# Performance work log

Measured on AMD Instinct MI355X. Metric: run time of the kernel, lower is better.

## Reference

```python
import jax, jax.numpy as jnp
import numpy as np

WS = 8          # window_size
NH = 8          # num_heads


def rel_pos_index(ws):
    coords = jnp.stack(jnp.meshgrid(jnp.arange(ws), jnp.arange(ws), indexing='ij'))  # [2,ws,ws]
    cf = coords.reshape(2, -1)                      # [2, N]
    rc = (cf[:, :, None] - cf[:, None, :]).transpose(1, 2, 0)  # [N,N,2]
    rc = rc + (ws - 1)
    return rc[..., 0] * (2 * ws - 1) + rc[..., 1]   # [N,N] int


def setup_inputs() -> dict:
    key = jax.random.key(0)
    ks = jax.random.split(key, 10)
    dim = 256
    B_, N = 4096, WS * WS
    nW = 1024
    return {
        'ref': jax.random.normal(ks[0], (B_, N, dim), jnp.float32),
        'adj': jax.random.normal(ks[1], (B_, N, dim), jnp.float32),
        'mask': jax.random.normal(ks[2], (nW, N, N), jnp.float32),
        'q_w': jax.random.normal(ks[3], (dim, dim), jnp.float32) * 0.02,
        'q_b': jax.random.normal(ks[4], (dim,), jnp.float32) * 0.02,
        'kv_w': jax.random.normal(ks[5], (2 * dim, dim), jnp.float32) * 0.02,
        'kv_b': jax.random.normal(ks[6], (2 * dim,), jnp.float32) * 0.02,
        'proj_w': jax.random.normal(ks[7], (dim, dim), jnp.float32) * 0.02,
        'proj_b': jax.random.normal(ks[8], (dim,), jnp.float32) * 0.02,
        'rpb_table': jax.random.normal(ks[9], ((2 * WS - 1) ** 2, NH), jnp.float32) * 0.02,
        'H': 256,
        'W': 256,
    }


def reference(ref, adj, mask, q_w, q_b, kv_w, kv_b, proj_w, proj_b, rpb_table, H, W):
    B_, N, C = ref.shape
    hd = C // NH
    scale = hd ** -0.5
    # projections (torch Linear: x @ W.T + b)
    q = (ref @ q_w.T + q_b).reshape(B_, N, NH, hd).transpose(0, 2, 1, 3)    # [B_,h,N,d]
    kv = (adj @ kv_w.T + kv_b).reshape(B_, N, 2, NH, hd)
    k = kv[:, :, 0].transpose(0, 2, 1, 3)                                   # [B_,h,N,d]
    v = kv[:, :, 1].transpose(0, 2, 1, 3)
    attn = jnp.einsum('bhnd,bhmd->bhnm', q * scale, k)                      # [B_,h,N,N]
    # relative position bias gather
    rpi = rel_pos_index(WS)                                                 # [N,N]
    bias = rpb_table[rpi.reshape(-1)].reshape(N, N, NH).transpose(2, 0, 1)  # [h,N,N]
    attn = attn + bias[None]
    # shifted-window mask
    nW = (H // WS) * (W // WS)
    attn = attn.reshape(B_ // nW, nW, NH, N, N) + mask[None, :, None]
    attn = attn.reshape(B_, NH, N, N)
    attn = jax.nn.softmax(attn, axis=-1)
    out = jnp.einsum('bhnm,bhmd->bhnd', attn, v).transpose(0, 2, 1, 3).reshape(B_, N, C)
    return out @ proj_w.T + proj_b
```

## Files before the change

### kernel.cpp

```cpp
#include <hip/hip_runtime.h>

typedef unsigned short u16;
typedef unsigned int u32;
typedef float f32x4 __attribute__((ext_vector_type(4)));
typedef __bf16 bf16x8 __attribute__((ext_vector_type(8)));

__device__ __forceinline__ u32 pack2(float a, float b) {
  u32 r;
  asm("v_cvt_pk_bf16_f32 %0, %1, %2" : "=v"(r) : "v"(a), "v"(b));
  return r;
}

__device__ __forceinline__ bf16x8 xpose_tile(const f32x4 t0, const f32x4 t1,
                                             int srcA, int srcB, bool hi) {
  u32 s0 = pack2(t0[0], t0[1]);
  u32 s1 = pack2(t0[2], t0[3]);
  u32 s2 = pack2(t1[0], t1[1]);
  u32 s3 = pack2(t1[2], t1[3]);
  u32 a00 = (u32)__shfl((int)s0, srcA), a20 = (u32)__shfl((int)s2, srcA);
  u32 a01 = (u32)__shfl((int)s1, srcA), a21 = (u32)__shfl((int)s3, srcA);
  u32 b00 = (u32)__shfl((int)s0, srcB), b20 = (u32)__shfl((int)s2, srcB);
  u32 b01 = (u32)__shfl((int)s1, srcB), b21 = (u32)__shfl((int)s3, srcB);
  uint4 u;
  u.x = hi ? a20 : a00;
  u.y = hi ? a21 : a01;
  u.z = hi ? b20 : b00;
  u.w = hi ? b21 : b01;
  return __builtin_bit_cast(bf16x8, u);
}

__global__ void prep_kern(const float* __restrict__ qw_f, const float* __restrict__ kvw_f,
                          const float* __restrict__ pjw_f, const float* __restrict__ rpb,
                          const float* __restrict__ mask_g,
                          uint4* __restrict__ qwt, uint4* __restrict__ kwt,
                          uint4* __restrict__ vwt, uint4* __restrict__ pjwt,
                          float4* __restrict__ biasT, float4* __restrict__ maskT, int nW) {
  int i = blockIdx.x * 256 + threadIdx.x;
  auto wxf = [&](const float* W, int ro, int idx, uint4* dst) {
    int l = idx & 63, kk = (idx >> 6) & 7, R = idx >> 9;
    const float* s = W + (ro + R * 16 + (l & 15)) * 256 + kk * 32 + 8 * (l >> 4);
    uint4 o;
    o.x = pack2(s[0], s[1]);
    o.y = pack2(s[2], s[3]);
    o.z = pack2(s[4], s[5]);
    o.w = pack2(s[6], s[7]);
    dst[idx] = o;
  };
  if (i < 32768) {
    wxf(qw_f, 0, i, qwt);
  } else if (i < 65536) {
    wxf(kvw_f, 0, i - 32768, kwt);
  } else if (i < 98304) {
    wxf(kvw_f, 256, i - 65536, vwt);
  } else if (i < 131072) {
    wxf(pjw_f, 0, i - 98304, pjwt);
  } else if (i < 139264) {
    int j = i - 131072;
    int l = j & 63, mt = (j >> 6) & 3, nt = (j >> 8) & 3, h = j >> 10;
    int n = nt * 16 + (l & 15), m0 = mt * 16 + 4 * (l >> 4);
    float4 o;
    float* po = (float*)&o;
#pragma unroll
    for (int e = 0; e < 4; ++e) {
      int m = m0 + e;
      int rp = ((n >> 3) - (m >> 3) + 7) * 15 + ((n & 7) - (m & 7) + 7);
      po[e] = rpb[rp * 8 + h];
    }
    biasT[j] = o;
  } else {
    int k = i - 139264;
    if (k < nW * 1024) {
      int l = k & 63, mt = (k >> 6) & 3, nt = (k >> 8) & 3, wd = k >> 10;
      int n = nt * 16 + (l & 15), m0 = mt * 16 + 4 * (l >> 4);
      maskT[k] = *(const float4*)(mask_g + (size_t)wd * 4096 + n * 64 + m0);
    }
  }
}

#define XROW 528

#define K1_LDS 67584

__global__ __launch_bounds__(256, 2) void winattn_kern(
    const float* __restrict__ xr_g, const float* __restrict__ xa_g,
    const float* __restrict__ qb_g, const float* __restrict__ kvb_g,
    const float* __restrict__ pb_g,
    const uint4* __restrict__ qwt, const uint4* __restrict__ kwt,
    const uint4* __restrict__ vwt, const uint4* __restrict__ pjwt,
    const float4* __restrict__ biasT, const float4* __restrict__ maskT,
    float* __restrict__ out_g, int nW) {
  extern __shared__ char smem[];
  const int tid = threadIdx.x;
  const int l = tid & 63, wv = tid >> 6;
  const int lr = l & 15, lq = l >> 4;
  const int b = blockIdx.x;
  const int wd = b % nW;
  const float scale = 0.17677669529663687f;
  const int srcA = lr + 32 * (lq & 1);
  const int srcB = srcA + 16;
  const bool hi = (lq >> 1) != 0;

  {
    const float* refb = xr_g + (size_t)b * 16384;
    const float* adjb = xa_g + (size_t)b * 16384;
#pragma unroll 4
    for (int it = 0; it < 16; ++it) {
      int flat = it * 256 + tid;
      int t = flat >> 6, c4 = (flat & 63) << 2;
      float4 vr = *(const float4*)(refb + t * 256 + c4);
      float4 va = *(const float4*)(adjb + t * 256 + c4);
      uint2 wr_, wa_;
      wr_.x = pack2(vr.x, vr.y);
      wr_.y = pack2(vr.z, vr.w);
      wa_.x = pack2(va.x, va.y);
      wa_.y = pack2(va.z, va.w);
      *(uint2*)(smem + t * XROW + c4 * 2) = wr_;
      *(uint2*)(smem + 33792 + t * XROW + c4 * 2) = wa_;
    }
  }
  __syncthreads();

  bf16x8 bfr[2][4], afr[2][4];

  {
    f32x4 qacc[4][4];
#pragma unroll
    for (int i = 0; i < 4; ++i)
#pragma unroll
      for (int j = 0; j < 4; ++j) qacc[i][j] = {0.f, 0.f, 0.f, 0.f};
#pragma unroll 2
    for (int kk = 0; kk < 8; ++kk) {
      bf16x8 a0 = *(const bf16x8*)&qwt[((wv * 4 + 0) * 8 + kk) * 64 + l];
      bf16x8 a1 = *(const bf16x8*)&qwt[((wv * 4 + 1) * 8 + kk) * 64 + l];
      bf16x8 a2 = *(const bf16x8*)&qwt[((wv * 4 + 2) * 8 + kk) * 64 + l];
      bf16x8 a3 = *(const bf16x8*)&qwt[((wv * 4 + 3) * 8 + kk) * 64 + l];
      int c = kk * 32 + 8 * lq;
#pragma unroll
      for (int nt = 0; nt < 4; ++nt) {
        bf16x8 bt = *(const bf16x8*)(smem + (nt * 16 + lr) * XROW + c * 2);
        qacc[0][nt] = __builtin_amdgcn_mfma_f32_16x16x32_bf16(a0, bt, qacc[0][nt], 0, 0, 0);
        qacc[1][nt] = __builtin_amdgcn_mfma_f32_16x16x32_bf16(a1, bt, qacc[1][nt], 0, 0, 0);
        qacc[2][nt] = __builtin_amdgcn_mfma_f32_16x16x32_bf16(a2, bt, qacc[2][nt], 0, 0, 0);
        qacc[3][nt] = __builtin_amdgcn_mfma_f32_16x16x32_bf16(a3, bt, qacc[3][nt], 0, 0, 0);
      }
    }
#pragma unroll
    for (int rt = 0; rt < 4; ++rt) {
      float4 b4 = *(const float4*)(qb_g + wv * 64 + rt * 16 + 4 * lq);
#pragma unroll
      for (int nt = 0; nt < 4; ++nt) {
        qacc[rt][nt][0] = (qacc[rt][nt][0] + b4.x) * scale;
        qacc[rt][nt][1] = (qacc[rt][nt][1] + b4.y) * scale;
        qacc[rt][nt][2] = (qacc[rt][nt][2] + b4.z) * scale;
        qacc[rt][nt][3] = (qacc[rt][nt][3] + b4.w) * scale;
      }
    }
#pragma unroll
    for (int h2 = 0; h2 < 2; ++h2)
#pragma unroll
      for (int nt = 0; nt < 4; ++nt)
        bfr[h2][nt] = xpose_tile(qacc[2 * h2][nt], qacc[2 * h2 + 1][nt], srcA, srcB, hi);
  }
  __syncthreads();

  {
    f32x4 kacc[4][4];
#pragma unroll
    for (int i = 0; i < 4; ++i)
#pragma unroll
      for (int j = 0; j < 4; ++j) kacc[i][j] = {0.f, 0.f, 0.f, 0.f};
#pragma unroll 2
    for (int kk = 0; kk < 8; ++kk) {
      bf16x8 a0 = *(const bf16x8*)&kwt[((wv * 4 + 0) * 8 + kk) * 64 + l];
      bf16x8 a1 = *(const bf16x8*)&kwt[((wv * 4 + 1) * 8 + kk) * 64 + l];
      bf16x8 a2 = *(const bf16x8*)&kwt[((wv * 4 + 2) * 8 + kk) * 64 + l];
      bf16x8 a3 = *(const bf16x8*)&kwt[((wv * 4 + 3) * 8 + kk) * 64 + l];
      int c = kk * 32 + 8 * lq;
#pragma unroll
      for (int nt = 0; nt < 4; ++nt) {
        bf16x8 bt = *(const bf16x8*)(smem + 33792 + (nt * 16 + lr) * XROW + c * 2);
        kacc[0][nt] = __builtin_amdgcn_mfma_f32_16x16x32_bf16(a0, bt, kacc[0][nt], 0, 0, 0);
        kacc[1][nt] = __builtin_amdgcn_mfma_f32_16x16x32_bf16(a1, bt, kacc[1][nt], 0, 0, 0);
        kacc[2][nt] = __builtin_amdgcn_mfma_f32_16x16x32_bf16(a2, bt, kacc[2][nt], 0, 0, 0);
        kacc[3][nt] = __builtin_amdgcn_mfma_f32_16x16x32_bf16(a3, bt, kacc[3][nt], 0, 0, 0);
      }
    }
#pragma unroll
    for (int rt = 0; rt < 4; ++rt) {
      float4 b4 = *(const float4*)(kvb_g + wv * 64 + rt * 16 + 4 * lq);
#pragma unroll
      for (int nt = 0; nt < 4; ++nt) {
        kacc[rt][nt][0] += b4.x;
        kacc[rt][nt][1] += b4.y;
        kacc[rt][nt][2] += b4.z;
        kacc[rt][nt][3] += b4.w;
      }
    }
#pragma unroll
    for (int h2 = 0; h2 < 2; ++h2)
#pragma unroll
      for (int nt = 0; nt < 4; ++nt)
        afr[h2][nt] = xpose_tile(kacc[2 * h2][nt], kacc[2 * h2 + 1][nt], srcA, srcB, hi);
  }

  bf16x8 vfr[2][2][2];
  {
    f32x4 vacc[4][4];
#pragma unroll
    for (int i = 0; i < 4; ++i)
#pragma unroll
      for (int j = 0; j < 4; ++j) vacc[i][j] = {0.f, 0.f, 0.f, 0.f};
#pragma unroll 2
    for (int kk = 0; kk < 8; ++kk) {
      bf16x8 b0 = *(const bf16x8*)&vwt[((wv * 4 + 0) * 8 + kk) * 64 + l];
      bf16x8 b1 = *(const bf16x8*)&vwt[((wv * 4 + 1) * 8 + kk) * 64 + l];
      bf16x8 b2 = *(const bf16x8*)&vwt[((wv * 4 + 2) * 8 + kk) * 64 + l];
      bf16x8 b3 = *(const bf16x8*)&vwt[((wv * 4 + 3) * 8 + kk) * 64 + l];
      int c = kk * 32 + 8 * lq;
#pragma unroll
      for (int mt = 0; mt < 4; ++mt) {
        bf16x8 at = *(const bf16x8*)(smem + 33792 + (mt * 16 + lr) * XROW + c * 2);
        vacc[mt][0] = __builtin_amdgcn_mfma_f32_16x16x32_bf16(at, b0, vacc[mt][0], 0, 0, 0);
        vacc[mt][1] = __builtin_amdgcn_mfma_f32_16x16x32_bf16(at, b1, vacc[mt][1], 0, 0, 0);
        vacc[mt][2] = __builtin_amdgcn_mfma_f32_16x16x32_bf16(at, b2, vacc[mt][2], 0, 0, 0);
        vacc[mt][3] = __builtin_amdgcn_mfma_f32_16x16x32_bf16(at, b3, vacc[mt][3], 0, 0, 0);
      }
    }
#pragma unroll
    for (int ct = 0; ct < 4; ++ct) {
      float bv = kvb_g[256 + wv * 64 + ct * 16 + lr];
#pragma unroll
      for (int mt = 0; mt < 4; ++mt)
#pragma unroll
        for (int j = 0; j < 4; ++j) vacc[mt][ct][j] += bv;
    }
#pragma unroll
    for (int h2 = 0; h2 < 2; ++h2)
#pragma unroll
      for (int kk = 0; kk < 2; ++kk)
#pragma unroll
        for (int cg = 0; cg < 2; ++cg)
          vfr[h2][kk][cg] =
              xpose_tile(vacc[2 * kk][2 * h2 + cg], vacc[2 * kk + 1][2 * h2 + cg], srcA, srcB, hi);
  }

#pragma unroll
  for (int h2 = 0; h2 < 2; ++h2) {
    const int h = wv * 2 + h2;

    f32x4 sacc[4][4];
    {
      const float4* bT = biasT + (size_t)h * 1024;
      const float4* mT = maskT + (size_t)wd * 1024;
#pragma unroll
      for (int nt = 0; nt < 4; ++nt) {
#pragma unroll
        for (int mt = 0; mt < 4; ++mt) {
          float4 bi = bT[(nt * 4 + mt) * 64 + l];
          float4 m4 = mT[(nt * 4 + mt) * 64 + l];
          sacc[mt][nt][0] = bi.x + m4.x;
          sacc[mt][nt][1] = bi.y + m4.y;
          sacc[mt][nt][2] = bi.z + m4.z;
          sacc[mt][nt][3] = bi.w + m4.w;
        }
      }
    }
#pragma unroll
    for (int mt = 0; mt < 4; ++mt)
#pragma unroll
      for (int nt = 0; nt < 4; ++nt)
        sacc[mt][nt] = __builtin_amdgcn_mfma_f32_16x16x32_bf16(afr[h2][mt], bfr[h2][nt],
                                                               sacc[mt][nt], 0, 0, 0);

    float rden[4];
#pragma unroll
    for (int nt = 0; nt < 4; ++nt) {
      float lmx = -1e30f;
#pragma unroll
      for (int mt = 0; mt < 4; ++mt)
        lmx = fmaxf(lmx, fmaxf(fmaxf(sacc[mt][nt][0], sacc[mt][nt][1]),
                               fmaxf(sacc[mt][nt][2], sacc[mt][nt][3])));
      lmx = fmaxf(lmx, __shfl_xor(lmx, 16));
      lmx = fmaxf(lmx, __shfl_xor(lmx, 32));
      float ls = 0.f;
#pragma unroll
      for (int mt = 0; mt < 4; ++mt) {
#pragma unroll
        for (int j = 0; j < 4; ++j) {
          float e = __expf(sacc[mt][nt][j] - lmx);
          sacc[mt][nt][j] = e;
          ls += e;
        }
      }
      ls += __shfl_xor(ls, 16);
      ls += __shfl_xor(ls, 32);
      rden[nt] = 1.0f / ls;
    }

    bf16x8 pfr[2][4];
#pragma unroll
    for (int kk = 0; kk < 2; ++kk)
#pragma unroll
      for (int nt = 0; nt < 4; ++nt)
        pfr[kk][nt] = xpose_tile(sacc[2 * kk][nt], sacc[2 * kk + 1][nt], srcA, srcB, hi);

    f32x4 oacc[2][4];
#pragma unroll
    for (int i = 0; i < 2; ++i)
#pragma unroll
      for (int j = 0; j < 4; ++j) oacc[i][j] = {0.f, 0.f, 0.f, 0.f};
#pragma unroll
    for (int kk = 0; kk < 2; ++kk)
#pragma unroll
      for (int nt = 0; nt < 4; ++nt) {
        oacc[0][nt] = __builtin_amdgcn_mfma_f32_16x16x32_bf16(vfr[h2][kk][0], pfr[kk][nt],
                                                              oacc[0][nt], 0, 0, 0);
        oacc[1][nt] = __builtin_amdgcn_mfma_f32_16x16x32_bf16(vfr[h2][kk][1], pfr[kk][nt],
                                                              oacc[1][nt], 0, 0, 0);
      }

#pragma unroll
    for (int cg = 0; cg < 2; ++cg) {
      int cb = h * 32 + cg * 16 + 4 * lq;
#pragma unroll
      for (int nt = 0; nt < 4; ++nt) {
        int n = nt * 16 + lr;
        float r = rden[nt];
        uint2 w;
        w.x = pack2(oacc[cg][nt][0] * r, oacc[cg][nt][1] * r);
        w.y = pack2(oacc[cg][nt][2] * r, oacc[cg][nt][3] * r);
        *(uint2*)(smem + n * XROW + cb * 2) = w;
      }
    }
  }
  __syncthreads();

  {
    f32x4 acc[4][4];
#pragma unroll
    for (int i = 0; i < 4; ++i)
#pragma unroll
      for (int j = 0; j < 4; ++j) acc[i][j] = {0.f, 0.f, 0.f, 0.f};
#pragma unroll 2
    for (int kk = 0; kk < 8; ++kk) {
      bf16x8 w0 = *(const bf16x8*)&pjwt[((wv * 4 + 0) * 8 + kk) * 64 + l];
      bf16x8 w1 = *(const bf16x8*)&pjwt[((wv * 4 + 1) * 8 + kk) * 64 + l];
      bf16x8 w2 = *(const bf16x8*)&pjwt[((wv * 4 + 2) * 8 + kk) * 64 + l];
      bf16x8 w3 = *(const bf16x8*)&pjwt[((wv * 4 + 3) * 8 + kk) * 64 + l];
      int c = kk * 32 + 8 * lq;
#pragma unroll
      for (int mt = 0; mt < 4; ++mt) {
        bf16x8 at = *(const bf16x8*)(smem + (mt * 16 + lr) * XROW + c * 2);
        acc[mt][0] = __builtin_amdgcn_mfma_f32_16x16x32_bf16(at, w0, acc[mt][0], 0, 0, 0);
        acc[mt][1] = __builtin_amdgcn_mfma_f32_16x16x32_bf16(at, w1, acc[mt][1], 0, 0, 0);
        acc[mt][2] = __builtin_amdgcn_mfma_f32_16x16x32_bf16(at, w2, acc[mt][2], 0, 0, 0);
        acc[mt][3] = __builtin_amdgcn_mfma_f32_16x16x32_bf16(at, w3, acc[mt][3], 0, 0, 0);
      }
    }
    float* outb = out_g + (size_t)b * 16384;
#pragma unroll
    for (int rt = 0; rt < 4; ++rt) {
      int c = wv * 64 + rt * 16 + lr;
      float pbv = pb_g[c];
#pragma unroll
      for (int mt = 0; mt < 4; ++mt) {
        int t = mt * 16 + 4 * lq;
        outb[(t + 0) * 256 + c] = acc[mt][rt][0] + pbv;
        outb[(t + 1) * 256 + c] = acc[mt][rt][1] + pbv;
        outb[(t + 2) * 256 + c] = acc[mt][rt][2] + pbv;
        outb[(t + 3) * 256 + c] = acc[mt][rt][3] + pbv;
      }
    }
  }
}

extern "C" void kernel_launch(void* const* d_in, const int* in_sizes, int n_in,
                              void* d_out, int out_size, void* d_ws, size_t ws_size,
                              hipStream_t stream) {
  const float* ref = (const float*)d_in[0];
  const float* adj = (const float*)d_in[1];
  const float* mask = (const float*)d_in[2];
  const float* q_w = (const float*)d_in[3];
  const float* q_b = (const float*)d_in[4];
  const float* kv_w = (const float*)d_in[5];
  const float* kv_b = (const float*)d_in[6];
  const float* proj_w = (const float*)d_in[7];
  const float* proj_b = (const float*)d_in[8];
  const float* rpb = (const float*)d_in[9];

  int B = in_sizes[0] / 16384;
  int nW = in_sizes[2] / 4096;

  uint4* qwt = (uint4*)d_ws;
  uint4* kwt = qwt + 32768;
  uint4* vwt = kwt + 32768;
  uint4* pjwt = vwt + 32768;
  float4* biasT = (float4*)(pjwt + 32768);
  float4* maskT = biasT + 8192;

  int prep_total = 139264 + nW * 1024;
  prep_kern<<<(prep_total + 255) / 256, 256, 0, stream>>>(q_w, kv_w, proj_w, rpb, mask, qwt,
                                                          kwt, vwt, pjwt, biasT, maskT, nW);

  hipFuncSetAttribute((const void*)winattn_kern, hipFuncAttributeMaxDynamicSharedMemorySize,
                      K1_LDS);
  winattn_kern<<<B, 256, K1_LDS, stream>>>(ref, adj, q_b, kv_b, proj_b, qwt, kwt, vwt, pjwt,
                                           biasT, maskT, (float*)d_out, nW);
}
```

Measured before the change: 316.7 us.

## Halve LDS footprint and split K/V per head to raise occupancy to three blocks

```diff
diff --git a/kernel.cpp b/kernel.cpp
--- a/kernel.cpp
+++ b/kernel.cpp
@@ -79,9 +79,9 @@
 
 #define XROW 528
 
-#define K1_LDS 67584
-
-__global__ __launch_bounds__(256, 2) void winattn_kern(
+#define K1_LDS 33792
+
+__global__ __launch_bounds__(256, 3) void winattn_kern(
     const float* __restrict__ xr_g, const float* __restrict__ xa_g,
     const float* __restrict__ qb_g, const float* __restrict__ kvb_g,
     const float* __restrict__ pb_g,
@@ -100,27 +100,23 @@
   const int srcB = srcA + 16;
   const bool hi = (lq >> 1) != 0;
 
-  {
-    const float* refb = xr_g + (size_t)b * 16384;
-    const float* adjb = xa_g + (size_t)b * 16384;
+  auto stage = [&](const float* src) {
 #pragma unroll 4
     for (int it = 0; it < 16; ++it) {
       int flat = it * 256 + tid;
       int t = flat >> 6, c4 = (flat & 63) << 2;
-      float4 vr = *(const float4*)(refb + t * 256 + c4);
-      float4 va = *(const float4*)(adjb + t * 256 + c4);
-      uint2 wr_, wa_;
-      wr_.x = pack2(vr.x, vr.y);
-      wr_.y = pack2(vr.z, vr.w);
-      wa_.x = pack2(va.x, va.y);
-      wa_.y = pack2(va.z, va.w);
-      *(uint2*)(smem + t * XROW + c4 * 2) = wr_;
-      *(uint2*)(smem + 33792 + t * XROW + c4 * 2) = wa_;
-    }
-  }
-  __syncthreads();
-
-  bf16x8 bfr[2][4], afr[2][4];
+      float4 v = *(const float4*)(src + t * 256 + c4);
+      uint2 w;
+      w.x = pack2(v.x, v.y);
+      w.y = pack2(v.z, v.w);
+      *(uint2*)(smem + t * XROW + c4 * 2) = w;
+    }
+  };
+
+  stage(xr_g + (size_t)b * 16384);
+  __syncthreads();
+
+  bf16x8 bfr[2][4];
 
   {
     f32x4 qacc[4][4];
@@ -163,174 +159,158 @@
   }
   __syncthreads();
 
+  stage(xa_g + (size_t)b * 16384);
+  __syncthreads();
+
+  uint2 po0[2][4];
+  f32x4 oacc1[2][4];
+  float rden1[4];
+
+#define KV_ATTN(H2, AFR, VFR, SACC, PFR, OACC, RDEN)                                          \
+  bf16x8 AFR[4];                                                                              \
+  {                                                                                           \
+    f32x4 kacc[2][4];                                                                         \
+    _Pragma("unroll") for (int i = 0; i < 2; ++i) _Pragma("unroll") for (int j = 0; j < 4;    \
+                                                                         ++j) kacc[i][j] = { \
+        0.f, 0.f, 0.f, 0.f};                                                                  \
+    _Pragma("unroll 2") for (int kk = 0; kk < 8; ++kk) {                                      \
+      bf16x8 a0 = *(const bf16x8*)&kwt[((wv * 4 + 2 * (H2) + 0) * 8 + kk) * 64 + l];          \
+      bf16x8 a1 = *(const bf16x8*)&kwt[((wv * 4 + 2 * (H2) + 1) * 8 + kk) * 64 + l];          \
+      int c = kk * 32 + 8 * lq;                                                               \
+      _Pragma("unroll") for (int nt = 0; nt < 4; ++nt) {                                      \
+        bf16x8 bt = *(const bf16x8*)(smem + (nt * 16 + lr) * XROW + c * 2);                   \
+        kacc[0][nt] = __builtin_amdgcn_mfma_f32_16x16x32_bf16(a0, bt, kacc[0][nt], 0, 0, 0);  \
+        kacc[1][nt] = __builtin_amdgcn_mfma_f32_16x16x32_bf16(a1, bt, kacc[1][nt], 0, 0, 0);  \
+      }                                                                                       \
+    }                                                                                         \
+    _Pragma("unroll") for (int r = 0; r < 2; ++r) {                                           \
+      float4 b4 = *(const float4*)(kvb_g + wv * 64 + (2 * (H2) + r) * 16 + 4 * lq);           \
+      _Pragma("unroll") for (int nt = 0; nt < 4; ++nt) {                                      \
+        kacc[r][nt][0] += b4.x;                                                               \
+        kacc[r][nt][1] += b4.y;                                                               \
+        kacc[r][nt][2] += b4.z;                                                               \
+        kacc[r][nt][3] += b4.w;                                                               \
+      }                                                                                       \
+    }                                                                                         \
+    _Pragma("unroll") for (int nt = 0; nt < 4; ++nt) AFR[nt] =                                \
+        xpose_tile(kacc[0][nt], kacc[1][nt], srcA, srcB, hi);                                 \
+  }                                                                                           \
+  bf16x8 VFR[2][2];                                                                           \
+  {                                                                                           \
+    f32x4 vacc[4][2];                                                                         \
+    _Pragma("unroll") for (int i = 0; i < 4; ++i) _Pragma("unroll") for (int j = 0; j < 2;    \
+                                                                         ++j) vacc[i][j] = { \
+        0.f, 0.f, 0.f, 0.f};                                                                  \
+    _Pragma("unroll 2") for (int kk = 0; kk < 8; ++kk) {                                      \
+      bf16x8 b0 = *(const bf16x8*)&vwt[((wv * 4 + 2 * (H2) + 0) * 8 + kk) * 64 + l];          \
+      bf16x8 b1 = *(const bf16x8*)&vwt[((wv * 4 + 2 * (H2) + 1) * 8 + kk) * 64 + l];          \
+      int c = kk * 32 + 8 * lq;                                                               \
+      _Pragma("unroll") for (int mt = 0; mt < 4; ++mt) {                                      \
+        bf16x8 at = *(const bf16x8*)(smem + (mt * 16 + lr) * XROW + c * 2);                   \
+        vacc[mt][0] = __builtin_amdgcn_mfma_f32_16x16x32_bf16(at, b0, vacc[mt][0], 0, 0, 0);  \
+        vacc[mt][1] = __builtin_amdgcn_mfma_f32_16x16x32_bf16(at, b1, vacc[mt][1], 0, 0, 0);  \
+      }                                                                                       \
+    }                                                                                         \
+    _Pragma("unroll") for (int cg = 0; cg < 2; ++cg) {                                        \
+      float bv = kvb_g[256 + wv * 64 + (2 * (H2) + cg) * 16 + lr];                            \
+      _Pragma("unroll") for (int mt = 0; mt < 4; ++mt) _Pragma("unroll") for (int j = 0;      \
+                                                                              j < 4; ++j)    \
+          vacc[mt][cg] += 0.f,                                                                \
+          vacc[mt][cg][j] += bv;                                                              \
+    }                                                                                         \
+    _Pragma("unroll") for (int kk = 0; kk < 2; ++kk) _Pragma("unroll") for (int cg = 0;       \
+                                                                            cg < 2; ++cg)    \
+        VFR[kk][cg] = xpose_tile(vacc[2 * kk][cg], vacc[2 * kk + 1][cg], srcA, srcB, hi);     \
+  }                                                                                           \
+  f32x4 SACC[4][4];                                                                           \
+  {                                                                                           \
+    const float4* bT = biasT + (size_t)(wv * 2 + (H2)) * 1024;                                \
+    const float4* mT = maskT + (size_t)wd * 1024;                                             \
+    _Pragma("unroll") for (int nt = 0; nt < 4; ++nt) _Pragma("unroll") for (int mt = 0;       \
+                                                                            mt < 4; ++mt) {  \
+      float4 bi = bT[(nt * 4 + mt) * 64 + l];                                                 \
+      float4 m4 = mT[(nt * 4 + mt) * 64 + l];                                                 \
+      SACC[mt][nt][0] = bi.x + m4.x;                                                          \
+      SACC[mt][nt][1] = bi.y + m4.y;                                                          \
+      SACC[mt][nt][2] = bi.z + m4.z;                                                          \
+      SACC[mt][nt][3] = bi.w + m4.w;                                                          \
+    }                                                                                         \
+  }                                                                                           \
+  _Pragma("unroll") for (int mt = 0; mt < 4; ++mt) _Pragma("unroll") for (int nt = 0; nt < 4; \
+                                                                          ++nt) SACC[mt]     \
+      [nt] = __builtin_amdgcn_mfma_f32_16x16x32_bf16(AFR[mt], bfr[H2][nt], SACC[mt][nt], 0,   \
+                                                     0, 0);                                   \
+  float RDEN[4];                                                                              \
+  _Pragma("unroll") for (int nt = 0; nt < 4; ++nt) {                                          \
+    float lmx = -1e30f;                                                                       \
+    _Pragma("unroll") for (int mt = 0; mt < 4; ++mt) lmx =                                    \
+        fmaxf(lmx, fmaxf(fmaxf(SACC[mt][nt][0], SACC[mt][nt][1]),                             \
+                         fmaxf(SACC[mt][nt][2], SACC[mt][nt][3])));                           \
+    lmx = fmaxf(lmx, __shfl_xor(lmx, 16));                                                    \
+    lmx = fmaxf(lmx, __shfl_xor(lmx, 32));                                                    \
+    float ls = 0.f;                                                                           \
+    _Pragma("unroll") for (int mt = 0; mt < 4; ++mt) _Pragma("unroll") for (int j = 0; j < 4; \
+                                                                            ++j) {           \
+      float e = __expf(SACC[mt][nt][j] - lmx);                                                \
+      SACC[mt][nt][j] = e;                                                                    \
+      ls += e;                                                                                \
+    }                                                                                         \
+    ls += __shfl_xor(ls, 16);                                                                 \
+    ls += __shfl_xor(ls, 32);                                                                 \
+    RDEN[nt] = 1.0f / ls;                                                                     \
+  }                                                                                           \
+  bf16x8 PFR[2][4];                                                                           \
+  _Pragma("unroll") for (int kk = 0; kk < 2; ++kk) _Pragma("unroll") for (int nt = 0; nt < 4; \
+                                                                          ++nt) PFR[kk]      \
+      [nt] = xpose_tile(SACC[2 * kk][nt], SACC[2 * kk + 1][nt], srcA, srcB, hi);              \
+  f32x4 OACC[2][4];                                                                           \
+  _Pragma("unroll") for (int i = 0; i < 2; ++i) _Pragma("unroll") for (int j = 0; j < 4; ++j) \
+      OACC[i][j] = {0.f, 0.f, 0.f, 0.f};                                                      \
+  _Pragma("unroll") for (int kk = 0; kk < 2; ++kk) _Pragma("unroll") for (int nt = 0; nt < 4; \
+                                                                          ++nt) {            \
+    OACC[0][nt] = __builtin_amdgcn_mfma_f32_16x16x32_bf16(VFR[kk][0], PFR[kk][nt],            \
+                                                          OACC[0][nt], 0, 0, 0);             \
+    OACC[1][nt] = __builtin_amdgcn_mfma_f32_16x16x32_bf16(VFR[kk][1], PFR[kk][nt],            \
+                                                          OACC[1][nt], 0, 0, 0);             \
+  }
+
   {
-    f32x4 kacc[4][4];
-#pragma unroll
-    for (int i = 0; i < 4; ++i)
-#pragma unroll
-      for (int j = 0; j < 4; ++j) kacc[i][j] = {0.f, 0.f, 0.f, 0.f};
-#pragma unroll 2
-    for (int kk = 0; kk < 8; ++kk) {
-      bf16x8 a0 = *(const bf16x8*)&kwt[((wv * 4 + 0) * 8 + kk) * 64 + l];
-      bf16x8 a1 = *(const bf16x8*)&kwt[((wv * 4 + 1) * 8 + kk) * 64 + l];
-      bf16x8 a2 = *(const bf16x8*)&kwt[((wv * 4 + 2) * 8 + kk) * 64 + l];
-      bf16x8 a3 = *(const bf16x8*)&kwt[((wv * 4 + 3) * 8 + kk) * 64 + l];
-      int c = kk * 32 + 8 * lq;
+    KV_ATTN(0, afr0, vfr0, sacc0, pfr0, oacc0, rden0)
+#pragma unroll
+    for (int cg = 0; cg < 2; ++cg)
 #pragma unroll
       for (int nt = 0; nt < 4; ++nt) {
-        bf16x8 bt = *(const bf16x8*)(smem + 33792 + (nt * 16 + lr) * XROW + c * 2);
-        kacc[0][nt] = __builtin_amdgcn_mfma_f32_16x16x32_bf16(a0, bt, kacc[0][nt], 0, 0, 0);
-        kacc[1][nt] = __builtin_amdgcn_mfma_f32_16x16x32_bf16(a1, bt, kacc[1][nt], 0, 0, 0);
-        kacc[2][nt] = __builtin_amdgcn_mfma_f32_16x16x32_bf16(a2, bt, kacc[2][nt], 0, 0, 0);
-        kacc[3][nt] = __builtin_amdgcn_mfma_f32_16x16x32_bf16(a3, bt, kacc[3][nt], 0, 0, 0);
-      }
-    }
-#pragma unroll
-    for (int rt = 0; rt < 4; ++rt) {
-      float4 b4 = *(const float4*)(kvb_g + wv * 64 + rt * 16 + 4 * lq);
-#pragma unroll
-      for (int nt = 0; nt < 4; ++nt) {
-        kacc[rt][nt][0] += b4.x;
-        kacc[rt][nt][1] += b4.y;
-        kacc[rt][nt][2] += b4.z;
-        kacc[rt][nt][3] += b4.w;
-      }
-    }
-#pragma unroll
-    for (int h2 = 0; h2 < 2; ++h2)
-#pragma unroll
-      for (int nt = 0; nt < 4; ++nt)
-        afr[h2][nt] = xpose_tile(kacc[2 * h2][nt], kacc[2 * h2 + 1][nt], srcA, srcB, hi);
-  }
-
-  bf16x8 vfr[2][2][2];
+        float r = rden0[nt];
+        po0[cg][nt].x = pack2(oacc0[cg][nt][0] * r, oacc0[cg][nt][1] * r);
+        po0[cg][nt].y = pack2(oacc0[cg][nt][2] * r, oacc0[cg][nt][3] * r);
+      }
+  }
   {
-    f32x4 vacc[4][4];
-#pragma unroll
-    for (int i = 0; i < 4; ++i)
-#pragma unroll
-      for (int j = 0; j < 4; ++j) vacc[i][j] = {0.f, 0.f, 0.f, 0.f};
-#pragma unroll 2
-    for (int kk = 0; kk < 8; ++kk) {
-      bf16x8 b0 = *(const bf16x8*)&vwt[((wv * 4 + 0) * 8 + kk) * 64 + l];
-      bf16x8 b1 = *(const bf16x8*)&vwt[((wv * 4 + 1) * 8 + kk) * 64 + l];
-      bf16x8 b2 = *(const bf16x8*)&vwt[((wv * 4 + 2) * 8 + kk) * 64 + l];
-      bf16x8 b3 = *(const bf16x8*)&vwt[((wv * 4 + 3) * 8 + kk) * 64 + l];
-      int c = kk * 32 + 8 * lq;
-#pragma unroll
-      for (int mt = 0; mt < 4; ++mt) {
-        bf16x8 at = *(const bf16x8*)(smem + 33792 + (mt * 16 + lr) * XROW + c * 2);
-        vacc[mt][0] = __builtin_amdgcn_mfma_f32_16x16x32_bf16(at, b0, vacc[mt][0], 0, 0, 0);
-        vacc[mt][1] = __builtin_amdgcn_mfma_f32_16x16x32_bf16(at, b1, vacc[mt][1], 0, 0, 0);
-        vacc[mt][2] = __builtin_amdgcn_mfma_f32_16x16x32_bf16(at, b2, vacc[mt][2], 0, 0, 0);
-        vacc[mt][3] = __builtin_amdgcn_mfma_f32_16x16x32_bf16(at, b3, vacc[mt][3], 0, 0, 0);
-      }
-    }
-#pragma unroll
-    for (int ct = 0; ct < 4; ++ct) {
-      float bv = kvb_g[256 + wv * 64 + ct * 16 + lr];
-#pragma unroll
-      for (int mt = 0; mt < 4; ++mt)
-#pragma unroll
-        for (int j = 0; j < 4; ++j) vacc[mt][ct][j] += bv;
-    }
-#pragma unroll
-    for (int h2 = 0; h2 < 2; ++h2)
-#pragma unroll
-      for (int kk = 0; kk < 2; ++kk)
-#pragma unroll
-        for (int cg = 0; cg < 2; ++cg)
-          vfr[h2][kk][cg] =
-              xpose_tile(vacc[2 * kk][2 * h2 + cg], vacc[2 * kk + 1][2 * h2 + cg], srcA, srcB, hi);
-  }
-
-#pragma unroll
-  for (int h2 = 0; h2 < 2; ++h2) {
-    const int h = wv * 2 + h2;
-
-    f32x4 sacc[4][4];
-    {
-      const float4* bT = biasT + (size_t)h * 1024;
-      const float4* mT = maskT + (size_t)wd * 1024;
-#pragma unroll
-      for (int nt = 0; nt < 4; ++nt) {
-#pragma unroll
-        for (int mt = 0; mt < 4; ++mt) {
-          float4 bi = bT[(nt * 4 + mt) * 64 + l];
-          float4 m4 = mT[(nt * 4 + mt) * 64 + l];
-          sacc[mt][nt][0] = bi.x + m4.x;
-          sacc[mt][nt][1] = bi.y + m4.y;
-          sacc[mt][nt][2] = bi.z + m4.z;
-          sacc[mt][nt][3] = bi.w + m4.w;
-        }
-      }
-    }
-#pragma unroll
-    for (int mt = 0; mt < 4; ++mt)
-#pragma unroll
-      for (int nt = 0; nt < 4; ++nt)
-        sacc[mt][nt] = __builtin_amdgcn_mfma_f32_16x16x32_bf16(afr[h2][mt], bfr[h2][nt],
-                                                               sacc[mt][nt], 0, 0, 0);
-
-    float rden[4];
+    KV_ATTN(1, afr1, vfr1, sacc1, pfr1, oaccT, rdenT)
+#pragma unroll
+    for (int i = 0; i < 2; ++i)
+#pragma unroll
+      for (int j = 0; j < 4; ++j) oacc1[i][j] = oaccT[i][j];
+#pragma unroll
+    for (int j = 0; j < 4; ++j) rden1[j] = rdenT[j];
+  }
+#undef KV_ATTN
+
+  __syncthreads();
+
+#pragma unroll
+  for (int cg = 0; cg < 2; ++cg) {
+    int cb0 = (wv * 2 + 0) * 32 + cg * 16 + 4 * lq;
+    int cb1 = (wv * 2 + 1) * 32 + cg * 16 + 4 * lq;
 #pragma unroll
     for (int nt = 0; nt < 4; ++nt) {
-      float lmx = -1e30f;
-#pragma unroll
-      for (int mt = 0; mt < 4; ++mt)
-        lmx = fmaxf(lmx, fmaxf(fmaxf(sacc[mt][nt][0], sacc[mt][nt][1]),
-                               fmaxf(sacc[mt][nt][2], sacc[mt][nt][3])));
-      lmx = fmaxf(lmx, __shfl_xor(lmx, 16));
-      lmx = fmaxf(lmx, __shfl_xor(lmx, 32));
-      float ls = 0.f;
-#pragma unroll
-      for (int mt = 0; mt < 4; ++mt) {
-#pragma unroll
-        for (int j = 0; j < 4; ++j) {
-          float e = __expf(sacc[mt][nt][j] - lmx);
-          sacc[mt][nt][j] = e;
-          ls += e;
-        }
-      }
-      ls += __shfl_xor(ls, 16);
-      ls += __shfl_xor(ls, 32);
-      rden[nt] = 1.0f / ls;
-    }
-
-    bf16x8 pfr[2][4];
-#pragma unroll
-    for (int kk = 0; kk < 2; ++kk)
-#pragma unroll
-      for (int nt = 0; nt < 4; ++nt)
-        pfr[kk][nt] = xpose_tile(sacc[2 * kk][nt], sacc[2 * kk + 1][nt], srcA, srcB, hi);
-
-    f32x4 oacc[2][4];
-#pragma unroll
-    for (int i = 0; i < 2; ++i)
-#pragma unroll
-      for (int j = 0; j < 4; ++j) oacc[i][j] = {0.f, 0.f, 0.f, 0.f};
-#pragma unroll
-    for (int kk = 0; kk < 2; ++kk)
-#pragma unroll
-      for (int nt = 0; nt < 4; ++nt) {
-        oacc[0][nt] = __builtin_amdgcn_mfma_f32_16x16x32_bf16(vfr[h2][kk][0], pfr[kk][nt],
-                                                              oacc[0][nt], 0, 0, 0);
-        oacc[1][nt] = __builtin_amdgcn_mfma_f32_16x16x32_bf16(vfr[h2][kk][1], pfr[kk][nt],
-                                                              oacc[1][nt], 0, 0, 0);
-      }
-
-#pragma unroll
-    for (int cg = 0; cg < 2; ++cg) {
-      int cb = h * 32 + cg * 16 + 4 * lq;
-#pragma unroll
-      for (int nt = 0; nt < 4; ++nt) {
-        int n = nt * 16 + lr;
-        float r = rden[nt];
-        uint2 w;
-        w.x = pack2(oacc[cg][nt][0] * r, oacc[cg][nt][1] * r);
-        w.y = pack2(oacc[cg][nt][2] * r, oacc[cg][nt][3] * r);
-        *(uint2*)(smem + n * XROW + cb * 2) = w;
-      }
+      int n = nt * 16 + lr;
+      *(uint2*)(smem + n * XROW + cb0 * 2) = po0[cg][nt];
+      float r = rden1[nt];
+      uint2 w1;
+      w1.x = pack2(oacc1[cg][nt][0] * r, oacc1[cg][nt][1] * r);
+      w1.y = pack2(oacc1[cg][nt][2] * r, oacc1[cg][nt][3] * r);
+      *(uint2*)(smem + n * XROW + cb1 * 2) = w1;
     }
   }
   __syncthreads();
```

Result: slower. 401.9 us (+26.9%).
